# Optimization experiments

Measured on AMD Instinct MI355X. Metric: run time of the kernel, lower is better.

The kernel has to match this reference:

```python
import jax, jax.numpy as jnp
import numpy as np

N_NODES = 100
F_IN = 65536
C_OUT = 60
ACTION_DIM = 100
N_EDGES = 2000


def setup_inputs() -> dict:
    key = jax.random.key(0)
    ks = jax.random.split(key, 16)
    s = 0.02
    return {
        "substrate_features": jax.random.normal(ks[0], (1, N_NODES, F_IN), jnp.float32),
        "edge_index": jax.random.randint(ks[1], (2, N_EDGES), 0, N_NODES, dtype=jnp.int32),
        "v_cpu_demand_t": jax.random.uniform(ks[2], (1,), jnp.float32),
        "v_bw_demand_t": jax.random.uniform(ks[3], (1,), jnp.float32),
        "num_pending_v_nodes_t": jax.random.uniform(ks[4], (1,), jnp.float32),
        "actor_w": jax.random.normal(ks[5], (3, F_IN, C_OUT), jnp.float32) * s,
        "actor_b": jax.random.normal(ks[6], (C_OUT,), jnp.float32) * s,
        "critic_w": jax.random.normal(ks[7], (3, F_IN, C_OUT), jnp.float32) * s,
        "critic_b": jax.random.normal(ks[8], (C_OUT,), jnp.float32) * s,
        "actor_fc_w": jax.random.normal(ks[9], (N_NODES * C_OUT + 3, ACTION_DIM), jnp.float32) * s,
        "actor_fc_b": jax.random.normal(ks[10], (ACTION_DIM,), jnp.float32) * s,
        "critic_fc_w": jax.random.normal(ks[11], (N_NODES * C_OUT + 3, 1), jnp.float32) * s,
        "critic_fc_b": jax.random.normal(ks[12], (1,), jnp.float32) * s,
    }


def cheb_conv(x, edge_index, W, b):
    # ChebConv, K=3, sym normalization, lambda_max=2 (PyG defaults).
    # With lambda_max=2 the scaled Laplacian is L_hat = -D^{-1/2} A D^{-1/2}
    # (diagonal becomes 0 after the -1 self-loop shift).
    # x: [1, N, F]; edge_index: [2, E]; W: [3, F, C]; b: [C]
    src, dst = edge_index[0], edge_index[1]
    n = x.shape[1]
    deg = jax.ops.segment_sum(jnp.ones(src.shape[0], x.dtype), src, num_segments=n)
    dis = jnp.where(deg > 0, jax.lax.rsqrt(jnp.where(deg > 0, deg, 1.0)), 0.0)
    norm = -(dis[src] * dis[dst])  # [E], L_hat off-diagonal entries
    x2 = x[0]  # [N, F]

    def prop(z):  # z: [N, F] -> L_hat @ z via gather/scatter over edges
        return jax.ops.segment_sum(z[src] * norm[:, None], dst, num_segments=n)

    Tx0 = x2
    Tx1 = prop(Tx0)
    Tx2 = 2.0 * prop(Tx1) - Tx0
    out = Tx0 @ W[0] + Tx1 @ W[1] + Tx2 @ W[2] + b  # [N, C]
    return out[None]  # [1, N, C]


def reference(substrate_features, edge_index, v_cpu_demand_t, v_bw_demand_t,
              num_pending_v_nodes_t, actor_w, actor_b, critic_w, critic_b,
              actor_fc_w, actor_fc_b, critic_fc_w, critic_fc_b):
    emb_a = jnp.tanh(cheb_conv(substrate_features, edge_index, actor_w, actor_b))
    emb_a = emb_a.reshape(1, -1)  # [1, N*60]
    emb_c = jnp.tanh(cheb_conv(substrate_features, edge_index, critic_w, critic_b))
    emb_c = emb_c.reshape(1, -1)
    extras = [v_cpu_demand_t[None], v_bw_demand_t[None], num_pending_v_nodes_t[None]]  # each [1,1]
    state_a = jnp.concatenate([emb_a] + extras, axis=1)  # [1, 6003]
    state_c = jnp.concatenate([emb_c] + extras, axis=1)
    logits = state_a @ actor_fc_w + actor_fc_b  # [1, action_dim]
    values = state_c @ critic_fc_w + critic_fc_b  # [1, 1]
    return (logits, values)
```

## Files before the change

kernel.cpp:

```cpp
#include <hip/hip_runtime.h>
#include <stdint.h>

#define F_IN 65536
#define NN 100
#define CO 60
#define G_SPLIT 256
#define KC (F_IN/G_SPLIT)
#define BK 32
#define NIT (KC/BK)

typedef short v8s __attribute__((ext_vector_type(8)));
typedef float v4f __attribute__((ext_vector_type(4)));

__device__ __forceinline__ unsigned int f2bf(float x){
  unsigned int u = __float_as_uint(x);
  u += 0x7fffu + ((u>>16)&1u);
  return u>>16;
}
__device__ __forceinline__ v4f mfma16(v8s a, v8s b, v4f c){
  return __builtin_amdgcn_mfma_f32_16x16x32_bf16(a,b,c,0,0,0);
}

__global__ __launch_bounds__(256)
void k_cvt(const float* __restrict__ x, unsigned short* __restrict__ xb){
  int i = blockIdx.x*256 + threadIdx.x;
  float4 v = ((const float4*)x)[i];
  uint2 w;
  w.x = f2bf(v.x) | (f2bf(v.y)<<16);
  w.y = f2bf(v.z) | (f2bf(v.w)<<16);
  ((uint2*)xb)[i] = w;
}

__global__ __launch_bounds__(256,4)
void k_gemm(const unsigned short* __restrict__ xb, const float* __restrict__ aw,
            const float* __restrict__ cw, float* __restrict__ dst, int partial){
  const int s = blockIdx.x, g = blockIdx.y;
  const int k0 = s*KC;
  const int tid = threadIdx.x, wave = tid>>6, lane = tid&63, quad = lane>>4, nl = lane&15;
  const int c0 = wave*16, ccl = min(c0+nl, CO-1);

  const float* Wm = (g<3) ? (aw + (size_t)g*F_IN*CO) : (cw + (size_t)(g-3)*F_IN*CO);
  const float* wp = Wm + (size_t)(k0 + quad*8)*CO + ccl;

  const unsigned short* ap[7];
  #pragma unroll
  for(int mt=0;mt<7;++mt){
    int r = mt*16 + nl;
    int rcl = min(r, NN-1);
    ap[mt] = xb + (size_t)rcl*F_IN + k0 + quad*8;
  }

  v4f acc[7];
  #pragma unroll
  for(int i=0;i<7;++i){ v4f z={0.f,0.f,0.f,0.f}; acc[i]=z; }

  for(int it=0; it<NIT; ++it){
    const int kk = it*BK;
    v8s a0 = *(const v8s*)(ap[0] + kk);
    v8s a1 = *(const v8s*)(ap[1] + kk);
    v8s a2 = *(const v8s*)(ap[2] + kk);
    v8s a3 = *(const v8s*)(ap[3] + kk);
    v8s a4 = *(const v8s*)(ap[4] + kk);
    v8s a5 = *(const v8s*)(ap[5] + kk);
    v8s a6 = *(const v8s*)(ap[6] + kk);
    float w0 = wp[(kk+0)*CO], w1 = wp[(kk+1)*CO], w2 = wp[(kk+2)*CO], w3 = wp[(kk+3)*CO];
    float w4 = wp[(kk+4)*CO], w5 = wp[(kk+5)*CO], w6 = wp[(kk+6)*CO], w7 = wp[(kk+7)*CO];
    v8s fB;
    fB[0]=(short)f2bf(w0); fB[1]=(short)f2bf(w1); fB[2]=(short)f2bf(w2); fB[3]=(short)f2bf(w3);
    fB[4]=(short)f2bf(w4); fB[5]=(short)f2bf(w5); fB[6]=(short)f2bf(w6); fB[7]=(short)f2bf(w7);
    acc[0] = mfma16(a0, fB, acc[0]);
    acc[1] = mfma16(a1, fB, acc[1]);
    acc[2] = mfma16(a2, fB, acc[2]);
    acc[3] = mfma16(a3, fB, acc[3]);
    acc[4] = mfma16(a4, fB, acc[4]);
    acc[5] = mfma16(a5, fB, acc[5]);
    acc[6] = mfma16(a6, fB, acc[6]);
  }

  const int c = c0 + nl;
  if(c < CO){
    if(partial){
      float* pd = dst + ((size_t)g*G_SPLIT + s)*(NN*CO);
      #pragma unroll
      for(int mt=0;mt<7;++mt){
        #pragma unroll
        for(int i=0;i<4;++i){
          int m = mt*16 + quad*4 + i;
          if(m < NN) pd[m*CO + c] = acc[mt][i];
        }
      }
    } else {
      float* pd = dst + (size_t)g*(NN*CO);
      #pragma unroll
      for(int mt=0;mt<7;++mt){
        #pragma unroll
        for(int i=0;i<4;++i){
          int m = mt*16 + quad*4 + i;
          if(m < NN) atomicAdd(pd + m*CO + c, acc[mt][i]);
        }
      }
    }
  }
}

__global__ void k_reduce(const float* __restrict__ P, float* __restrict__ Y){
  int o = blockIdx.x*256 + threadIdx.x;
  if(o >= 6*NN*CO) return;
  int gg = o/(NN*CO), r = o - gg*(NN*CO);
  const float* p = P + (size_t)gg*G_SPLIT*(NN*CO) + (size_t)blockIdx.y*32*(NN*CO) + r;
  float a0=0.f,a1=0.f,a2=0.f,a3=0.f;
  #pragma unroll 2
  for(int s4=0;s4<32;s4+=4){
    a0 += p[(s4  )*(NN*CO)];
    a1 += p[(s4+1)*(NN*CO)];
    a2 += p[(s4+2)*(NN*CO)];
    a3 += p[(s4+3)*(NN*CO)];
  }
  atomicAdd(&Y[o], (a0+a1)+(a2+a3));
}

__global__ void k_cheb(const float* __restrict__ Y, const int* __restrict__ ei,
                       const float* __restrict__ ab, const float* __restrict__ cb,
                       float* __restrict__ emb){
  const int net = blockIdx.x / CO;
  const int c   = blockIdx.x % CO;
  const int t   = threadIdx.x;
  __shared__ float L[NN][NN+1];
  __shared__ float dis[NN];
  __shared__ int   deg[NN];
  __shared__ float y0[NN], y1[NN], y2[NN], zu[NN];

  for(int i=t;i<NN*(NN+1);i+=128) ((float*)L)[i]=0.f;
  if(t<NN) deg[t]=0;
  __syncthreads();
  for(int e=t;e<2000;e+=128) atomicAdd(&deg[ei[e]],1);
  __syncthreads();
  if(t<NN) dis[t] = deg[t]>0 ? rsqrtf((float)deg[t]) : 0.f;
  __syncthreads();
  for(int e=t;e<2000;e+=128){
    int s = ei[e], d = ei[2000+e];
    atomicAdd(&L[d][s], -dis[s]*dis[d]);
  }
  if(t<NN){
    const float* yb = Y + (size_t)net*3*NN*CO + t*CO + c;
    y0[t]=yb[0]; y1[t]=yb[NN*CO]; y2[t]=yb[2*NN*CO];
  }
  __syncthreads();
  if(t<NN){
    float s=0.f;
    #pragma unroll 4
    for(int j=0;j<NN;++j) s += L[t][j]*y2[j];
    zu[t] = y1[t] + 2.f*s;
  }
  __syncthreads();
  if(t<NN){
    float s=0.f;
    #pragma unroll 4
    for(int j=0;j<NN;++j) s += L[t][j]*zu[j];
    float b = (net==0) ? ab[c] : cb[c];
    emb[net*NN*CO + t*CO + c] = tanhf(y0[t] - y2[t] + s + b);
  }
}

#define FCB 25
__global__ void k_fc(const float* __restrict__ emb, const float* __restrict__ afw,
                     const float* __restrict__ afb, const float* __restrict__ cfw,
                     const float* __restrict__ cfb, const float* __restrict__ s0,
                     const float* __restrict__ s1, const float* __restrict__ s2,
                     float* __restrict__ out){
  const int b = blockIdx.x;
  const int t = threadIdx.x;
  if(b < FCB){
    const int jj = t & 127, half = t >> 7;
    if(jj < 100){
      const int i0 = b*240 + half*120;
      const float* w = afw + (size_t)i0*100 + jj;
      const float* e = emb + i0;
      float p = 0.f;
      #pragma unroll 4
      for(int i=0;i<120;++i) p += e[i]*w[(size_t)i*100];
      atomicAdd(&out[jj], p);
    }
  } else {
    float p = 0.f;
    const float* e = emb + 6000;
    for(int i=t;i<6000;i+=256) p += e[i]*cfw[i];
    #pragma unroll
    for(int o=32;o>0;o>>=1) p += __shfl_down(p,o,64);
    __shared__ float red[4];
    if((t&63)==0) red[t>>6]=p;
    __syncthreads();
    if(t==0){
      float tot = red[0]+red[1]+red[2]+red[3];
      out[100] = tot + s0[0]*cfw[6000] + s1[0]*cfw[6001] + s2[0]*cfw[6002] + cfb[0];
    }
    if(t<100){
      atomicAdd(&out[t], afb[t] + s0[0]*afw[600000+t] + s1[0]*afw[600100+t] + s2[0]*afw[600200+t]);
    }
  }
}

extern "C" void kernel_launch(void* const* d_in, const int* in_sizes, int n_in,
                              void* d_out, int out_size, void* d_ws, size_t ws_size,
                              hipStream_t stream){
  const float* x   = (const float*)d_in[0];
  const int*   ei  = (const int*)d_in[1];
  const float* s0  = (const float*)d_in[2];
  const float* s1  = (const float*)d_in[3];
  const float* s2  = (const float*)d_in[4];
  const float* aw  = (const float*)d_in[5];
  const float* ab  = (const float*)d_in[6];
  const float* cw  = (const float*)d_in[7];
  const float* cb  = (const float*)d_in[8];
  const float* afw = (const float*)d_in[9];
  const float* afb = (const float*)d_in[10];
  const float* cfw = (const float*)d_in[11];
  const float* cfb = (const float*)d_in[12];
  float* out = (float*)d_out;

  unsigned short* xb = (unsigned short*)d_ws;
  float* Y   = (float*)((char*)d_ws + 13107200);
  float* emb = Y + 6*NN*CO;
  float* P   = emb + 2*NN*CO;
  const size_t need_full = 13107200u + (size_t)(6*NN*CO + 2*NN*CO)*4
                         + (size_t)6*G_SPLIT*NN*CO*4;
  const int partial = (ws_size >= need_full) ? 1 : 0;

  hipMemsetAsync(Y, 0, 6*NN*CO*sizeof(float), stream);
  hipMemsetAsync(out, 0, 101*sizeof(float), stream);

  k_cvt<<<6400, 256, 0, stream>>>(x, xb);
  k_gemm<<<dim3(G_SPLIT,6), 256, 0, stream>>>(xb, aw, cw, partial ? P : Y, partial);
  if(partial){
    k_reduce<<<dim3((6*NN*CO+255)/256, 8), 256, 0, stream>>>(P, Y);
  }
  k_cheb<<<120, 128, 0, stream>>>(Y, ei, ab, cb, emb);
  k_fc<<<FCB+1, 256, 0, stream>>>(emb, afw, afb, cfw, cfb, s0, s1, s2, out);
}
```

Baseline: 243.3 us.

## Fuse bf16 conversion of x into GEMM via LDS staging and prefetch weights

Drops the separate fp32-to-bf16 conversion kernel and its 13 MB bf16 workspace. Each GEMM block now loads its own K-slice of x, converts it, and stages it in shared memory for the MFMA A operands. Weight loads are double-buffered with inline-asm global loads and explicit vmcnt waits, and the loop is fully unrolled. Occupancy hint drops to 2 blocks per CU because of the ~59 KB LDS tile. Each of the six g-blocks re-reads the same fp32 x slice, so x traffic goes up in exchange for removing a kernel launch and a write/read round trip.

Measured after the change: 223.4 us. 8.2% less time.

```diff
diff --git a/kernel.cpp b/kernel.cpp
--- a/kernel.cpp
+++ b/kernel.cpp
@@ -8,6 +8,7 @@
 #define KC (F_IN/G_SPLIT)
 #define BK 32
 #define NIT (KC/BK)
+#define AROW 264
 
 typedef short v8s __attribute__((ext_vector_type(8)));
 typedef float v4f __attribute__((ext_vector_type(4)));
@@ -21,18 +22,30 @@
   return __builtin_amdgcn_mfma_f32_16x16x32_bf16(a,b,c,0,0,0);
 }
 
-__global__ __launch_bounds__(256)
-void k_cvt(const float* __restrict__ x, unsigned short* __restrict__ xb){
-  int i = blockIdx.x*256 + threadIdx.x;
-  float4 v = ((const float4*)x)[i];
-  uint2 w;
-  w.x = f2bf(v.x) | (f2bf(v.y)<<16);
-  w.y = f2bf(v.z) | (f2bf(v.w)<<16);
-  ((uint2*)xb)[i] = w;
-}
-
-__global__ __launch_bounds__(256,4)
-void k_gemm(const unsigned short* __restrict__ xb, const float* __restrict__ aw,
+#define LOADB(BNK_, ITN_) \
+  asm volatile( \
+    "global_load_dword %0, %8, %9\n\t" \
+    "global_load_dword %1, %8, %9 offset:240\n\t" \
+    "global_load_dword %2, %8, %9 offset:480\n\t" \
+    "global_load_dword %3, %8, %9 offset:720\n\t" \
+    "global_load_dword %4, %8, %9 offset:960\n\t" \
+    "global_load_dword %5, %8, %9 offset:1200\n\t" \
+    "global_load_dword %6, %8, %9 offset:1440\n\t" \
+    "global_load_dword %7, %8, %9 offset:1680\n\t" \
+    : "=&v"(Bb[(BNK_)][0]), "=&v"(Bb[(BNK_)][1]), "=&v"(Bb[(BNK_)][2]), \
+      "=&v"(Bb[(BNK_)][3]), "=&v"(Bb[(BNK_)][4]), "=&v"(Bb[(BNK_)][5]), \
+      "=&v"(Bb[(BNK_)][6]), "=&v"(Bb[(BNK_)][7]) \
+    : "v"(wo + (ITN_)*7680u), "s"(Wm) \
+    : )
+
+#define WAITB(BNK_, CNT_) \
+  asm volatile("s_waitcnt vmcnt(" CNT_ ")" \
+    : "+v"(Bb[(BNK_)][0]), "+v"(Bb[(BNK_)][1]), "+v"(Bb[(BNK_)][2]), \
+      "+v"(Bb[(BNK_)][3]), "+v"(Bb[(BNK_)][4]), "+v"(Bb[(BNK_)][5]), \
+      "+v"(Bb[(BNK_)][6]), "+v"(Bb[(BNK_)][7]) :: )
+
+__global__ __launch_bounds__(256,2)
+void k_gemm(const float* __restrict__ x, const float* __restrict__ aw,
             const float* __restrict__ cw, float* __restrict__ dst, int partial){
   const int s = blockIdx.x, g = blockIdx.y;
   const int k0 = s*KC;
@@ -40,41 +53,49 @@
   const int c0 = wave*16, ccl = min(c0+nl, CO-1);
 
   const float* Wm = (g<3) ? (aw + (size_t)g*F_IN*CO) : (cw + (size_t)(g-3)*F_IN*CO);
-  const float* wp = Wm + (size_t)(k0 + quad*8)*CO + ccl;
-
-  const unsigned short* ap[7];
+  const unsigned int wo = (unsigned)(((k0 + quad*8)*CO + ccl)*4);
+
+  __shared__ __align__(16) unsigned short As[112*AROW];
+
   #pragma unroll
-  for(int mt=0;mt<7;++mt){
-    int r = mt*16 + nl;
-    int rcl = min(r, NN-1);
-    ap[mt] = xb + (size_t)rcl*F_IN + k0 + quad*8;
-  }
-
+  for(int p=0;p<28;++p){
+    int lin = p*256 + tid;
+    int row = lin>>6, ch = lin&63;
+    int rcl = min(row, NN-1);
+    float4 v = *(const float4*)(x + (size_t)rcl*F_IN + k0 + ch*4);
+    uint2 w;
+    w.x = f2bf(v.x) | (f2bf(v.y)<<16);
+    w.y = f2bf(v.z) | (f2bf(v.w)<<16);
+    *(uint2*)((char*)As + row*528 + ch*8) = w;
+  }
+  __syncthreads();
+
+  float Bb[2][8];
   v4f acc[7];
   #pragma unroll
   for(int i=0;i<7;++i){ v4f z={0.f,0.f,0.f,0.f}; acc[i]=z; }
 
+  LOADB(0, 0);
+
+  const char* Abase = (const char*)As + nl*528 + quad*16;
+
+  #pragma unroll
   for(int it=0; it<NIT; ++it){
-    const int kk = it*BK;
-    v8s a0 = *(const v8s*)(ap[0] + kk);
-    v8s a1 = *(const v8s*)(ap[1] + kk);
-    v8s a2 = *(const v8s*)(ap[2] + kk);
-    v8s a3 = *(const v8s*)(ap[3] + kk);
-    v8s a4 = *(const v8s*)(ap[4] + kk);
-    v8s a5 = *(const v8s*)(ap[5] + kk);
-    v8s a6 = *(const v8s*)(ap[6] + kk);
-    float w0 = wp[(kk+0)*CO], w1 = wp[(kk+1)*CO], w2 = wp[(kk+2)*CO], w3 = wp[(kk+3)*CO];
-    float w4 = wp[(kk+4)*CO], w5 = wp[(kk+5)*CO], w6 = wp[(kk+6)*CO], w7 = wp[(kk+7)*CO];
+    if(it+1 < NIT){
+      LOADB((it+1)&1, it+1);
+      WAITB(it&1, "8");
+    } else {
+      WAITB(it&1, "0");
+    }
+    const int bk = it&1;
     v8s fB;
-    fB[0]=(short)f2bf(w0); fB[1]=(short)f2bf(w1); fB[2]=(short)f2bf(w2); fB[3]=(short)f2bf(w3);
-    fB[4]=(short)f2bf(w4); fB[5]=(short)f2bf(w5); fB[6]=(short)f2bf(w6); fB[7]=(short)f2bf(w7);
-    acc[0] = mfma16(a0, fB, acc[0]);
-    acc[1] = mfma16(a1, fB, acc[1]);
-    acc[2] = mfma16(a2, fB, acc[2]);
-    acc[3] = mfma16(a3, fB, acc[3]);
-    acc[4] = mfma16(a4, fB, acc[4]);
-    acc[5] = mfma16(a5, fB, acc[5]);
-    acc[6] = mfma16(a6, fB, acc[6]);
+    #pragma unroll
+    for(int j=0;j<8;++j) fB[j] = (short)f2bf(Bb[bk][j]);
+    #pragma unroll
+    for(int mt=0;mt<7;++mt){
+      v8s a = *(const v8s*)(Abase + mt*8448 + it*64);
+      acc[mt] = mfma16(a, fB, acc[mt]);
+    }
   }
 
   const int c = c0 + nl;
@@ -218,19 +239,16 @@
   const float* cfb = (const float*)d_in[12];
   float* out = (float*)d_out;
 
-  unsigned short* xb = (unsigned short*)d_ws;
-  float* Y   = (float*)((char*)d_ws + 13107200);
+  float* P   = (float*)d_ws;
+  float* Y   = P + (size_t)6*G_SPLIT*NN*CO;
   float* emb = Y + 6*NN*CO;
-  float* P   = emb + 2*NN*CO;
-  const size_t need_full = 13107200u + (size_t)(6*NN*CO + 2*NN*CO)*4
-                         + (size_t)6*G_SPLIT*NN*CO*4;
+  const size_t need_full = ((size_t)6*G_SPLIT*NN*CO + 6*NN*CO + 2*NN*CO)*sizeof(float);
   const int partial = (ws_size >= need_full) ? 1 : 0;
 
   hipMemsetAsync(Y, 0, 6*NN*CO*sizeof(float), stream);
   hipMemsetAsync(out, 0, 101*sizeof(float), stream);
 
-  k_cvt<<<6400, 256, 0, stream>>>(x, xb);
-  k_gemm<<<dim3(G_SPLIT,6), 256, 0, stream>>>(xb, aw, cw, partial ? P : Y, partial);
+  k_gemm<<<dim3(G_SPLIT,6), 256, 0, stream>>>(x, aw, cw, partial ? P : Y, partial);
   if(partial){
     k_reduce<<<dim3((6*NN*CO+255)/256, 8), 256, 0, stream>>>(P, Y);
   }
```
